# Kernel optimization log

Hardware: AMD Instinct MI355X
Metric: run time of the kernel (lower is better)

## Reference

```python
import jax, jax.numpy as jnp
import numpy as np

N_ENTITY = 100000
N_RELATION = 64
DIM = 64
N_LAYER = 2
BATCH = 4096
N_TRIPLES = 128


def setup_inputs() -> dict:
    key = jax.random.key(0)
    ks = jax.random.split(key, 9)
    ts = (N_LAYER, BATCH, N_TRIPLES)
    return {
        "items": jax.random.randint(ks[0], (BATCH,), 0, N_ENTITY),
        "user_h": jax.random.randint(ks[1], ts, 0, N_ENTITY),
        "user_r": jax.random.randint(ks[2], ts, 0, N_RELATION),
        "user_t": jax.random.randint(ks[3], ts, 0, N_ENTITY),
        "item_h": jax.random.randint(ks[4], ts, 0, N_ENTITY),
        "item_r": jax.random.randint(ks[5], ts, 0, N_RELATION),
        "item_t": jax.random.randint(ks[6], ts, 0, N_ENTITY),
        "entity_emb": jax.random.normal(ks[7], (N_ENTITY, DIM), jnp.float32),
        "relation_emb": jax.random.normal(ks[8], (N_RELATION, DIM), jnp.float32),
    }


def _sim_attention(h_emb, t_emb, anchor):
    # h_emb, t_emb: [B, T, D]; anchor: [B, D]
    sim = jnp.einsum("btd,bd->bt", h_emb, anchor)      # dot-product similarity
    w = jax.nn.softmax(sim, axis=-1)                    # softmax over triple set
    return jnp.einsum("bt,btd->bd", w, t_emb)           # weighted sum of tails


def reference(items, user_h, user_r, user_t, item_h, item_r, item_t,
              entity_emb, relation_emb):
    # item side
    item_origin = entity_emb[items]                     # [B, D]
    e_v = item_origin
    for i in range(N_LAYER):
        h = entity_emb[item_h[i]]                       # [B, T, D]
        t = entity_emb[item_t[i]]
        e_v = e_v + _sim_attention(h, t, item_origin)   # agg == 'sum'
    # user side
    user_0 = entity_emb[user_h[0]].mean(axis=1)         # [B, D]
    e_u = user_0
    for i in range(N_LAYER):
        h = entity_emb[user_h[i]]
        t = entity_emb[user_t[i]]
        e_u = e_u + _sim_attention(h, t, user_0)
    scores = jax.nn.sigmoid(jnp.sum(e_v * e_u, axis=1))  # [B]
    return scores
```

## Files before the change

kernel.cpp:

```cpp
#include <hip/hip_runtime.h>
#include <hip/hip_fp16.h>

#define BATCH 4096
#define NTRI  128
#define DIM   64
#define NENT  100000
#define WTH   1e-5f

typedef int   v2i __attribute__((ext_vector_type(2)));
typedef float v4f __attribute__((ext_vector_type(4)));

struct Smem {
    int   idx[4][2 * NTRI];
    int   meanidx[NTRI];
    float simw[4][NTRI];
    int   cidx[4][NTRI];
    float cw[4][NTRI];
    float res[4][DIM];
    float anch_u[DIM];
    float anch_v[DIM];
};

__global__ __launch_bounds__(256) void convert_fp16(
    const float* __restrict__ src, __half* __restrict__ dst, int n8) {
    const int i = blockIdx.x * 256 + threadIdx.x;
    if (i >= n8) return;
    const v4f a = __builtin_nontemporal_load((const v4f*)src + 2 * i);
    const v4f b = __builtin_nontemporal_load((const v4f*)src + 2 * i + 1);
    __half2 h0 = __floats2half2_rn(a.x, a.y);
    __half2 h1 = __floats2half2_rn(a.z, a.w);
    __half2 h2 = __floats2half2_rn(b.x, b.y);
    __half2 h3 = __floats2half2_rn(b.z, b.w);
    uint4 o;
    o.x = *(const unsigned*)&h0;
    o.y = *(const unsigned*)&h1;
    o.z = *(const unsigned*)&h2;
    o.w = *(const unsigned*)&h3;
    ((uint4*)dst)[i] = o;
}

__device__ __forceinline__ void load8(const __half* __restrict__ p, float f[8]) {
    const uint4 r = *(const uint4*)p;
    float2 q;
    q = __half22float2(*(const __half2*)&r.x); f[0] = q.x; f[1] = q.y;
    q = __half22float2(*(const __half2*)&r.y); f[2] = q.x; f[3] = q.y;
    q = __half22float2(*(const __half2*)&r.z); f[4] = q.x; f[5] = q.y;
    q = __half22float2(*(const __half2*)&r.w); f[6] = q.x; f[7] = q.y;
}

__device__ __forceinline__ void bfly8(float f[8], int m) {
#pragma unroll
    for (int j = 0; j < 8; ++j) f[j] += __shfl_xor(f[j], m, 64);
}

__global__ __launch_bounds__(256) void KCDN_67997922230517_kernel(
    const int* __restrict__ items,
    const int* __restrict__ user_h, const int* __restrict__ user_t,
    const int* __restrict__ item_h, const int* __restrict__ item_t,
    const float* __restrict__ ent, const __half* __restrict__ tab,
    float* __restrict__ out) {
    __shared__ __align__(16) Smem sm;
    const int b    = blockIdx.x;
    const int tid  = threadIdx.x;
    const int w    = tid >> 6;
    const int lane = tid & 63;
    const int oct  = lane >> 3;
    const int ol   = lane & 7;
    const int dstart = ol * 8;

    {
        const int* hsrc; const int* tsrc; size_t off;
        if (w == 0)      { hsrc = user_h; tsrc = user_t; off = (size_t)b * NTRI; }
        else if (w == 1) { hsrc = user_h; tsrc = user_t; off = ((size_t)BATCH + b) * NTRI; }
        else if (w == 2) { hsrc = item_h; tsrc = item_t; off = (size_t)b * NTRI; }
        else             { hsrc = item_h; tsrc = item_t; off = ((size_t)BATCH + b) * NTRI; }
        *(v2i*)(&sm.idx[w][lane * 2]) =
            __builtin_nontemporal_load((const v2i*)(hsrc + off + lane * 2));
        *(v2i*)(&sm.idx[w][NTRI + lane * 2]) =
            __builtin_nontemporal_load((const v2i*)(tsrc + off + lane * 2));
        if (w == 1)
            *(v2i*)(&sm.meanidx[lane * 2]) =
                __builtin_nontemporal_load((const v2i*)(user_h + (size_t)b * NTRI + lane * 2));
    }

    float anc[8];
    if (w >= 2) {
        const int it = __builtin_nontemporal_load(items + b);
        const size_t ii = (size_t)it * DIM + dstart;
        const v4f a0 = __builtin_nontemporal_load((const v4f*)(ent + ii));
        const v4f a1 = __builtin_nontemporal_load((const v4f*)(ent + ii + 4));
        anc[0] = a0.x; anc[1] = a0.y; anc[2] = a0.z; anc[3] = a0.w;
        anc[4] = a1.x; anc[5] = a1.y; anc[6] = a1.z; anc[7] = a1.w;
    } else {
        const int* mi = (w == 0) ? sm.idx[0] : sm.meanidx;
        float a[8] = {0, 0, 0, 0, 0, 0, 0, 0};
#pragma unroll 4
        for (int k = 0; k < 16; ++k) {
            const int e = oct * 16 + k;
            const size_t id = (size_t)mi[e];
            float f[8]; load8(tab + id * DIM + dstart, f);
#pragma unroll
            for (int j = 0; j < 8; ++j) a[j] += f[j];
        }
        bfly8(a, 8); bfly8(a, 16); bfly8(a, 32);
#pragma unroll
        for (int j = 0; j < 8; ++j) anc[j] = a[j] * (1.0f / 128.0f);
    }
    if (w == 0 && lane < 8) {
#pragma unroll
        for (int j = 0; j < 8; ++j) sm.anch_u[dstart + j] = anc[j];
    }
    if (w == 2 && lane < 8) {
#pragma unroll
        for (int j = 0; j < 8; ++j) sm.anch_v[dstart + j] = anc[j];
    }

#pragma unroll 4
    for (int k = 0; k < 16; ++k) {
        const int e = oct * 16 + k;
        const size_t id = (size_t)sm.idx[w][e];
        float f[8]; load8(tab + id * DIM + dstart, f);
        float v = f[0] * anc[0] + f[1] * anc[1] + f[2] * anc[2] + f[3] * anc[3]
                + f[4] * anc[4] + f[5] * anc[5] + f[6] * anc[6] + f[7] * anc[7];
        v += __shfl_xor(v, 1, 64);
        v += __shfl_xor(v, 2, 64);
        v += __shfl_xor(v, 4, 64);
        if (ol == 0) sm.simw[w][k * 8 + oct] = v;
    }

    {
        float v0 = sm.simw[w][lane];
        float v1 = sm.simw[w][lane + 64];
        float m = fmaxf(v0, v1);
#pragma unroll
        for (int off = 32; off; off >>= 1) m = fmaxf(m, __shfl_xor(m, off, 64));
        const float e0 = __expf(v0 - m), e1 = __expf(v1 - m);
        float s = e0 + e1;
#pragma unroll
        for (int off = 32; off; off >>= 1) s += __shfl_xor(s, off, 64);
        const float inv = 1.0f / s;
        sm.simw[w][lane]      = e0 * inv;
        sm.simw[w][lane + 64] = e1 * inv;
    }

    int nkeep;
    {
        const float w0 = sm.simw[w][lane];
        const float w1 = sm.simw[w][lane + 64];
        const int s0 = ((lane & 7) << 4) | (lane >> 3);
        const int s1 = ((lane & 7) << 4) | ((lane >> 3) + 8);
        const bool k0 = w0 > WTH, k1 = w1 > WTH;
        const unsigned long long b0 = __ballot(k0);
        const unsigned long long b1 = __ballot(k1);
        const int c0 = __popcll(b0);
        const unsigned long long below = (1ull << lane) - 1ull;
        const int p0 = __popcll(b0 & below);
        const int p1 = c0 + __popcll(b1 & below);
        if (k0) { sm.cidx[w][p0] = sm.idx[w][NTRI + s0]; sm.cw[w][p0] = w0; }
        if (k1) { sm.cidx[w][p1] = sm.idx[w][NTRI + s1]; sm.cw[w][p1] = w1; }
        nkeep = c0 + __popcll(b1);
    }

    float acc[8] = {0, 0, 0, 0, 0, 0, 0, 0};
    for (int e = oct; e < nkeep; e += 8) {
        const size_t id = (size_t)sm.cidx[w][e];
        const float wt = sm.cw[w][e];
        float f[8]; load8(tab + id * DIM + dstart, f);
#pragma unroll
        for (int j = 0; j < 8; ++j) acc[j] += wt * f[j];
    }
    bfly8(acc, 8); bfly8(acc, 16); bfly8(acc, 32);
    if (lane < 8) {
#pragma unroll
        for (int j = 0; j < 8; ++j) sm.res[w][dstart + j] = acc[j];
    }

    __syncthreads();

    if (tid < 64) {
        const float eu = sm.anch_u[tid] + sm.res[0][tid] + sm.res[1][tid];
        const float ev = sm.anch_v[tid] + sm.res[2][tid] + sm.res[3][tid];
        float v = eu * ev;
#pragma unroll
        for (int off = 32; off; off >>= 1) v += __shfl_xor(v, off, 64);
        if (tid == 0) out[b] = 1.0f / (1.0f + __expf(-v));
    }
}

extern "C" void kernel_launch(void* const* d_in, const int* in_sizes, int n_in,
                              void* d_out, int out_size, void* d_ws, size_t ws_size,
                              hipStream_t stream) {
    const int*   items  = (const int*)d_in[0];
    const int*   user_h = (const int*)d_in[1];
    const int*   user_t = (const int*)d_in[3];
    const int*   item_h = (const int*)d_in[4];
    const int*   item_t = (const int*)d_in[6];
    const float* ent    = (const float*)d_in[7];
    float*       out    = (float*)d_out;
    __half*      tab    = (__half*)d_ws;

    const int n8 = NENT * DIM / 8;
    hipLaunchKernelGGL(convert_fp16, dim3((n8 + 255) / 256), dim3(256), 0, stream,
                       ent, tab, n8);
    hipLaunchKernelGGL(KCDN_67997922230517_kernel, dim3(BATCH), dim3(256), 0, stream,
                       items, user_h, user_t, item_h, item_t, ent, tab, out);
}
```

Measured before the change: 150.6 us.

## Prefetch user-side tail embeddings early and drop weight compaction for user waves

```diff
diff --git a/kernel.cpp b/kernel.cpp
--- a/kernel.cpp
+++ b/kernel.cpp
@@ -14,8 +14,8 @@
     int   idx[4][2 * NTRI];
     int   meanidx[NTRI];
     float simw[4][NTRI];
-    int   cidx[4][NTRI];
-    float cw[4][NTRI];
+    int   cidx[2][NTRI];
+    float cw[2][NTRI];
     float res[4][DIM];
     float anch_u[DIM];
     float anch_v[DIM];
@@ -39,8 +39,7 @@
     ((uint4*)dst)[i] = o;
 }
 
-__device__ __forceinline__ void load8(const __half* __restrict__ p, float f[8]) {
-    const uint4 r = *(const uint4*)p;
+__device__ __forceinline__ void cvt8(const uint4 r, float f[8]) {
     float2 q;
     q = __half22float2(*(const __half2*)&r.x); f[0] = q.x; f[1] = q.y;
     q = __half22float2(*(const __half2*)&r.y); f[2] = q.x; f[3] = q.y;
@@ -48,17 +47,20 @@
     q = __half22float2(*(const __half2*)&r.w); f[6] = q.x; f[7] = q.y;
 }
 
+__device__ __forceinline__ void load8(const __half* __restrict__ p, float f[8]) {
+    cvt8(*(const uint4*)p, f);
+}
+
 __device__ __forceinline__ void bfly8(float f[8], int m) {
 #pragma unroll
     for (int j = 0; j < 8; ++j) f[j] += __shfl_xor(f[j], m, 64);
 }
 
-__global__ __launch_bounds__(256) void KCDN_67997922230517_kernel(
+__global__ __launch_bounds__(256, 4) void KCDN_67997922230517_kernel(
     const int* __restrict__ items,
     const int* __restrict__ user_h, const int* __restrict__ user_t,
     const int* __restrict__ item_h, const int* __restrict__ item_t,
-    const float* __restrict__ ent, const __half* __restrict__ tab,
-    float* __restrict__ out) {
+    const __half* __restrict__ tab, float* __restrict__ out) {
     __shared__ __align__(16) Smem sm;
     const int b    = blockIdx.x;
     const int tid  = threadIdx.x;
@@ -83,18 +85,23 @@
                 __builtin_nontemporal_load((const v2i*)(user_h + (size_t)b * NTRI + lane * 2));
     }
 
+    uint4 tpre[8];
+    if (w < 2) {
+#pragma unroll
+        for (int k = 0; k < 8; ++k) {
+            const size_t id = (size_t)sm.idx[w][NTRI + oct * 16 + k];
+            tpre[k] = *(const uint4*)(tab + id * DIM + dstart);
+        }
+    }
+
     float anc[8];
     if (w >= 2) {
         const int it = __builtin_nontemporal_load(items + b);
-        const size_t ii = (size_t)it * DIM + dstart;
-        const v4f a0 = __builtin_nontemporal_load((const v4f*)(ent + ii));
-        const v4f a1 = __builtin_nontemporal_load((const v4f*)(ent + ii + 4));
-        anc[0] = a0.x; anc[1] = a0.y; anc[2] = a0.z; anc[3] = a0.w;
-        anc[4] = a1.x; anc[5] = a1.y; anc[6] = a1.z; anc[7] = a1.w;
+        load8(tab + (size_t)it * DIM + dstart, anc);
     } else {
         const int* mi = (w == 0) ? sm.idx[0] : sm.meanidx;
         float a[8] = {0, 0, 0, 0, 0, 0, 0, 0};
-#pragma unroll 4
+#pragma unroll 8
         for (int k = 0; k < 16; ++k) {
             const int e = oct * 16 + k;
             const size_t id = (size_t)mi[e];
@@ -115,7 +122,7 @@
         for (int j = 0; j < 8; ++j) sm.anch_v[dstart + j] = anc[j];
     }
 
-#pragma unroll 4
+#pragma unroll 8
     for (int k = 0; k < 16; ++k) {
         const int e = oct * 16 + k;
         const size_t id = (size_t)sm.idx[w][e];
@@ -143,31 +150,54 @@
         sm.simw[w][lane + 64] = e1 * inv;
     }
 
-    int nkeep;
-    {
-        const float w0 = sm.simw[w][lane];
-        const float w1 = sm.simw[w][lane + 64];
-        const int s0 = ((lane & 7) << 4) | (lane >> 3);
-        const int s1 = ((lane & 7) << 4) | ((lane >> 3) + 8);
-        const bool k0 = w0 > WTH, k1 = w1 > WTH;
-        const unsigned long long b0 = __ballot(k0);
-        const unsigned long long b1 = __ballot(k1);
-        const int c0 = __popcll(b0);
-        const unsigned long long below = (1ull << lane) - 1ull;
-        const int p0 = __popcll(b0 & below);
-        const int p1 = c0 + __popcll(b1 & below);
-        if (k0) { sm.cidx[w][p0] = sm.idx[w][NTRI + s0]; sm.cw[w][p0] = w0; }
-        if (k1) { sm.cidx[w][p1] = sm.idx[w][NTRI + s1]; sm.cw[w][p1] = w1; }
-        nkeep = c0 + __popcll(b1);
-    }
-
     float acc[8] = {0, 0, 0, 0, 0, 0, 0, 0};
-    for (int e = oct; e < nkeep; e += 8) {
-        const size_t id = (size_t)sm.cidx[w][e];
-        const float wt = sm.cw[w][e];
-        float f[8]; load8(tab + id * DIM + dstart, f);
-#pragma unroll
-        for (int j = 0; j < 8; ++j) acc[j] += wt * f[j];
+    if (w < 2) {
+        uint4 t2[8];
+#pragma unroll
+        for (int k = 0; k < 8; ++k) {
+            const size_t id = (size_t)sm.idx[w][NTRI + oct * 16 + 8 + k];
+            t2[k] = *(const uint4*)(tab + id * DIM + dstart);
+        }
+#pragma unroll
+        for (int k = 0; k < 8; ++k) {
+            const float wt = sm.simw[w][k * 8 + oct];
+            float f[8]; cvt8(tpre[k], f);
+#pragma unroll
+            for (int j = 0; j < 8; ++j) acc[j] += wt * f[j];
+        }
+#pragma unroll
+        for (int k = 0; k < 8; ++k) {
+            const float wt = sm.simw[w][(8 + k) * 8 + oct];
+            float f[8]; cvt8(t2[k], f);
+#pragma unroll
+            for (int j = 0; j < 8; ++j) acc[j] += wt * f[j];
+        }
+    } else {
+        const int cs = w - 2;
+        int nkeep;
+        {
+            const float w0 = sm.simw[w][lane];
+            const float w1 = sm.simw[w][lane + 64];
+            const int s0 = ((lane & 7) << 4) | (lane >> 3);
+            const int s1 = ((lane & 7) << 4) | ((lane >> 3) + 8);
+            const bool k0 = w0 > WTH, k1 = w1 > WTH;
+            const unsigned long long b0 = __ballot(k0);
+            const unsigned long long b1 = __ballot(k1);
+            const int c0 = __popcll(b0);
+            const unsigned long long below = (1ull << lane) - 1ull;
+            const int p0 = __popcll(b0 & below);
+            const int p1 = c0 + __popcll(b1 & below);
+            if (k0) { sm.cidx[cs][p0] = sm.idx[w][NTRI + s0]; sm.cw[cs][p0] = w0; }
+            if (k1) { sm.cidx[cs][p1] = sm.idx[w][NTRI + s1]; sm.cw[cs][p1] = w1; }
+            nkeep = c0 + __popcll(b1);
+        }
+        for (int e = oct; e < nkeep; e += 8) {
+            const size_t id = (size_t)sm.cidx[cs][e];
+            const float wt = sm.cw[cs][e];
+            float f[8]; load8(tab + id * DIM + dstart, f);
+#pragma unroll
+            for (int j = 0; j < 8; ++j) acc[j] += wt * f[j];
+        }
     }
     bfly8(acc, 8); bfly8(acc, 16); bfly8(acc, 32);
     if (lane < 8) {
@@ -203,5 +233,5 @@
     hipLaunchKernelGGL(convert_fp16, dim3((n8 + 255) / 256), dim3(256), 0, stream,
                        ent, tab, n8);
     hipLaunchKernelGGL(KCDN_67997922230517_kernel, dim3(BATCH), dim3(256), 0, stream,
-                       items, user_h, user_t, item_h, item_t, ent, tab, out);
-}
+                       items, user_h, user_t, item_h, item_t, tab, out);
+}
```

New measurement: 158.2 us. +5.1%, slower.
